# Optimization experiments

Measured on AMD Instinct MI355X. Metric: run time of the kernel, lower is better.

The kernel has to match this reference:

```python
import jax, jax.numpy as jnp
import numpy as np

TEMP = 10.0  # softmax_ called with N=10.0 in reduce_func

def qmul(a, b):
    # Hamilton product, rows are (w, x, y, z)
    aw, ax, ay, az = a[..., 0], a[..., 1], a[..., 2], a[..., 3]
    bw, bx, by, bz = b[..., 0], b[..., 1], b[..., 2], b[..., 3]
    return jnp.stack([
        aw * bw - ax * bx - ay * by - az * bz,
        aw * bx + ax * bw + ay * bz - az * by,
        aw * by - ax * bz + ay * bw + az * bx,
        aw * bz + ax * by - ay * bx + az * bw,
    ], axis=-1)

def setup_inputs() -> dict:
    key = jax.random.key(0)
    k1, k2, k3, k4, k5, k6 = jax.random.split(key, 6)
    N, E = 100000, 3200000
    node_levels = jax.random.uniform(k1, (N,), dtype=jnp.float32)
    node_q = jax.random.normal(k2, (N, 4), dtype=jnp.float32)
    node_q = node_q / jnp.linalg.norm(node_q, axis=1, keepdims=True)
    edge_rel_q = jax.random.normal(k3, (E, 4), dtype=jnp.float32)
    edge_rel_q = edge_rel_q / jnp.linalg.norm(edge_rel_q, axis=1, keepdims=True)
    edge_w = jax.random.uniform(k4, (E,), dtype=jnp.float32)
    src = jax.random.randint(k5, (E,), 0, N, dtype=jnp.int32)
    dst = jax.random.randint(k6, (E,), 0, N, dtype=jnp.int32)
    return {"node_levels": node_levels, "node_q": node_q,
            "edge_rel_q": edge_rel_q, "edge_w": edge_w,
            "src": src, "dst": dst}

def reference(node_levels, node_q, edge_rel_q, edge_w, src, dst):
    N = node_q.shape[0]
    # per-edge message: accumulated quaternion rel_q * q_src
    accu_q = qmul(edge_rel_q, node_q[src])          # [E,4]
    l_src = node_levels[src]                        # [E]
    # softmax logits: cost = w * l (self term has w = 1)
    cost_e = TEMP * edge_w * l_src                  # [E]
    cost_self = TEMP * node_levels                  # [N]
    # segmented stable softmax over {self} U in-edges per dst node
    seg_max = jax.ops.segment_max(cost_e, dst, num_segments=N)
    m = jnp.maximum(seg_max, cost_self)             # [N]
    exp_e = jnp.exp(cost_e - m[dst])                # [E]
    exp_self = jnp.exp(cost_self - m)               # [N]
    Z = jax.ops.segment_sum(exp_e, dst, num_segments=N) + exp_self
    # weighted sums
    sum_q = jax.ops.segment_sum(exp_e[:, None] * accu_q, dst, num_segments=N) \
            + exp_self[:, None] * node_q            # [N,4]
    sum_l = jax.ops.segment_sum(exp_e * l_src, dst, num_segments=N) \
            + exp_self * node_levels                # [N]
    out_q = sum_q / Z[:, None]
    out_levels = sum_l / Z
    # F.normalize(q, p=2, dim=1) with eps=1e-12 clamp
    norm = jnp.maximum(jnp.linalg.norm(out_q, axis=1, keepdims=True), 1e-12)
    return out_q / norm, out_levels
```

## Files before the change

kernel.cpp:

```cpp
#include <hip/hip_runtime.h>
#include <hip/hip_fp16.h>

#define TEMP 10.0f
#define TPB 512
#define HTPB 256
#define NBLK 768
#define SHIFT 9
#define GSZ 512
#define BMAX 256
#define TILE 2048
#define GTPB 1024
#define CAP 44

typedef float v2f  __attribute__((ext_vector_type(2)));
typedef float vf4  __attribute__((ext_vector_type(4)));
typedef unsigned uv4 __attribute__((ext_vector_type(4)));

__device__ __forceinline__ int   nt_i (const int* p)   { return __builtin_nontemporal_load(p); }
__device__ __forceinline__ float nt_f (const float* p) { return __builtin_nontemporal_load(p); }
__device__ __forceinline__ float4 nt_f4(const float4* p) {
    vf4 v = __builtin_nontemporal_load((const vf4*)p);
    return make_float4(v.x, v.y, v.z, v.w);
}
__device__ __forceinline__ uint4 nt_u4(const uint4* p) {
    uv4 v = __builtin_nontemporal_load((const uv4*)p);
    uint4 r; r.x = v.x; r.y = v.y; r.z = v.z; r.w = v.w; return r;
}

__device__ __forceinline__ void pk_fadd(float* p, float a, float b) {
#if __has_builtin(__builtin_amdgcn_global_atomic_fadd_v2f32)
    v2f v; v.x = a; v.y = b;
    __builtin_amdgcn_global_atomic_fadd_v2f32(
        (__attribute__((address_space(1))) v2f*)p, v);
#else
    atomicAdd(p, a); atomicAdd(p + 1, b);
#endif
}

__device__ __forceinline__ void hamilton(float4 a, float4 b,
                                         float& ow, float& ox, float& oy, float& oz) {
    ow = a.x*b.x - a.y*b.y - a.z*b.z - a.w*b.w;
    ox = a.x*b.y + a.y*b.x + a.z*b.w - a.w*b.z;
    oy = a.x*b.z - a.y*b.w + a.z*b.x + a.w*b.y;
    oz = a.x*b.w + a.y*b.z - a.z*b.y + a.w*b.x;
}

__device__ __forceinline__ unsigned f2h(float x) {
    return (unsigned)__half_as_ushort(__float2half_rn(x));
}
__device__ __forceinline__ float h2f(unsigned u) {
    return __half2float(__ushort_as_half((unsigned short)(u & 0xFFFFu)));
}

__global__ void __launch_bounds__(HTPB)
hist_kernel(const int* __restrict__ dst, unsigned* __restrict__ blkhist,
            int E, int B, int span) {
    extern __shared__ unsigned h[];
    for (int i = threadIdx.x; i < B; i += blockDim.x) h[i] = 0;
    __syncthreads();
    int start = blockIdx.x * span;
    int end = start + span; if (end > E) end = E;
    for (int e = start + threadIdx.x; e < end; e += blockDim.x)
        atomicAdd(&h[((unsigned)nt_i(&dst[e])) >> SHIFT], 1u);
    __syncthreads();
    for (int i = threadIdx.x; i < B; i += blockDim.x)
        blkhist[(size_t)i * gridDim.x + blockIdx.x] = h[i];
}

__global__ void __launch_bounds__(1024)
scan_blocks_kernel(unsigned* __restrict__ blkhist, unsigned* __restrict__ totals) {
    __shared__ unsigned s[1024];
    int b = blockIdx.x, t = threadIdx.x, n = blockDim.x;
    unsigned v = blkhist[(size_t)b * n + t];
    s[t] = v; __syncthreads();
    for (int off = 1; off < n; off <<= 1) {
        unsigned add = (t >= off) ? s[t - off] : 0u;
        __syncthreads();
        s[t] += add;
        __syncthreads();
    }
    blkhist[(size_t)b * n + t] = s[t] - v;
    if (t == n - 1) totals[b] = s[t];
}

__global__ void __launch_bounds__(1024)
scan_totals_kernel(const unsigned* __restrict__ totals,
                   unsigned* __restrict__ offsets, int B) {
    __shared__ unsigned s[1024];
    int t = threadIdx.x;
    unsigned v = (t < B) ? totals[t] : 0u;
    s[t] = v; __syncthreads();
    for (int off = 1; off < 1024; off <<= 1) {
        unsigned add = (t >= off) ? s[t - off] : 0u;
        __syncthreads();
        s[t] += add;
        __syncthreads();
    }
    if (t < B) offsets[t] = s[t] - v;
    if (t == B - 1) offsets[B] = s[t];
}

__global__ void __launch_bounds__(TPB)
scatter_sort_kernel(const float* __restrict__ nl, const float4* __restrict__ nq,
                    const float4* __restrict__ erq, const float* __restrict__ ew,
                    const int* __restrict__ src, const int* __restrict__ dst,
                    const unsigned* __restrict__ blkhist,
                    const unsigned* __restrict__ offsets,
                    uint4* __restrict__ buckets,
                    int E, int B, int span) {
    __shared__ uint4    stage[TILE];
    __shared__ unsigned gslot[TILE];
    __shared__ unsigned gcur[BMAX];
    __shared__ unsigned th[BMAX];
    __shared__ unsigned basec[BMAX];
    __shared__ unsigned curt[BMAX];

    int blk = blockIdx.x, nb = gridDim.x, tid = threadIdx.x;
    for (int b = tid; b < B; b += TPB)
        gcur[b] = offsets[b] + blkhist[(size_t)b * nb + blk];
    int start = blk * span;
    int end = start + span; if (end > E) end = E;

    for (int ts = start; ts < end; ts += TILE) {
        int tE = end - ts; if (tE > TILE) tE = TILE;
        for (int b = tid; b < B; b += TPB) th[b] = 0;
        __syncthreads();
        for (int k = tid; k < tE; k += TPB)
            atomicAdd(&th[((unsigned)dst[ts + k]) >> SHIFT], 1u);
        __syncthreads();
        if (tid < 64) {
            int lane = tid;
            unsigned vals[4];
            unsigned tot = 0;
            #pragma unroll
            for (int c = 0; c < 4; ++c) {
                int i = lane * 4 + c;
                vals[c] = (i < B) ? th[i] : 0u;
                tot += vals[c];
            }
            unsigned inc = tot;
            #pragma unroll
            for (int off = 1; off < 64; off <<= 1) {
                unsigned up = __shfl_up(inc, off);
                if (lane >= off) inc += up;
            }
            unsigned run = inc - tot;
            #pragma unroll
            for (int c = 0; c < 4; ++c) {
                int i = lane * 4 + c;
                if (i < B) { basec[i] = run; curt[i] = run; }
                run += vals[c];
            }
        }
        __syncthreads();
        for (int k = tid; k < tE; k += TPB) {
            int e = ts + k;
            int s_ = nt_i(&src[e]);
            unsigned d = (unsigned)dst[e];
            float l = nl[s_];
            float p = __expf(TEMP * nt_f(&ew[e]) * l);
            float ow, ox, oy, oz;
            hamilton(nt_f4(&erq[e]), nq[s_], ow, ox, oy, oz);
            unsigned b = d >> SHIFT;
            unsigned pos = atomicAdd(&curt[b], 1u);
            uint4 pk;
            pk.x = (d & (GSZ - 1)) | (f2h(p) << 16);
            pk.y = f2h(p * l)  | (f2h(p * ow) << 16);
            pk.z = f2h(p * ox) | (f2h(p * oy) << 16);
            pk.w = f2h(p * oz);
            stage[pos] = pk;
            gslot[pos] = gcur[b] + (pos - basec[b]);
        }
        __syncthreads();
        for (int k = tid; k < tE; k += TPB)
            buckets[gslot[k]] = stage[k];
        __syncthreads();
        for (int b = tid; b < B; b += TPB) gcur[b] += th[b];
        __syncthreads();
    }
}

__global__ void __launch_bounds__(GTPB)
gather_pay_kernel(const float* __restrict__ nl, const float4* __restrict__ nq,
                  const unsigned* __restrict__ offsets,
                  const uint4* __restrict__ buckets,
                  float4* __restrict__ out_q, float* __restrict__ out_l, int N) {
    __shared__ unsigned short idx[GSZ * CAP];
    __shared__ int   curn[GSZ];
    __shared__ float ovf[GSZ * 7];
    int b = blockIdx.x, tid = threadIdx.x;
    for (int i = tid; i < GSZ; i += GTPB) curn[i] = 0;
    for (int i = tid; i < GSZ * 7; i += GTPB) ovf[i] = 0.f;
    __syncthreads();

    unsigned s0 = offsets[b], s1 = offsets[b + 1];
    int M = (int)(s1 - s0);
    const unsigned* bx = (const unsigned*)(buckets + s0);

    for (int i = tid; i < M; i += GTPB) {
        unsigned w0 = bx[4 * (size_t)i];
        unsigned dl = w0 & (GSZ - 1);
        int slot = atomicAdd(&curn[dl], 1);
        if (slot < CAP) {
            idx[dl * CAP + slot] = (unsigned short)i;
        } else {
            uint4 pk = buckets[s0 + i];
            float* a = &ovf[dl * 7];
            atomicAdd(a + 0, h2f(pk.x >> 16));
            atomicAdd(a + 1, h2f(pk.y));
            atomicAdd(a + 2, h2f(pk.y >> 16));
            atomicAdd(a + 3, h2f(pk.z));
            atomicAdd(a + 4, h2f(pk.z >> 16));
            atomicAdd(a + 5, h2f(pk.w));
        }
    }
    __syncthreads();

    for (int half = 0; half < (GSZ * 4) / GTPB; ++half) {
        int j = half * (GTPB / 4) + (tid >> 2);
        int r = tid & 3;
        int deg = curn[j]; if (deg > CAP) deg = CAP;
        float aZ = 0.f, aL = 0.f, a0 = 0.f, a1 = 0.f, a2 = 0.f, a3 = 0.f;
        for (int s = r; s < deg; s += 4) {
            int i = idx[j * CAP + s];
            uint4 pk = nt_u4(&buckets[s0 + i]);
            aZ += h2f(pk.x >> 16);
            aL += h2f(pk.y);
            a0 += h2f(pk.y >> 16);
            a1 += h2f(pk.z);
            a2 += h2f(pk.z >> 16);
            a3 += h2f(pk.w);
        }
        for (int m = 1; m <= 2; m <<= 1) {
            aZ += __shfl_xor(aZ, m); aL += __shfl_xor(aL, m);
            a0 += __shfl_xor(a0, m); a1 += __shfl_xor(a1, m);
            a2 += __shfl_xor(a2, m); a3 += __shfl_xor(a3, m);
        }
        if (r == 0) {
            int n = b * GSZ + j;
            if (n < N) {
                const float* o = &ovf[j * 7];
                float l = nl[n];
                float ps = __expf(TEMP * l);
                float Z  = aZ + o[0] + ps;
                float sl = aL + o[1] + ps * l;
                float4 q = nq[n];
                float qw = a0 + o[2] + ps * q.x;
                float qx = a1 + o[3] + ps * q.y;
                float qy = a2 + o[4] + ps * q.z;
                float qz = a3 + o[5] + ps * q.w;
                float inv = 1.0f / Z;
                qw *= inv; qx *= inv; qy *= inv; qz *= inv;
                float norm = fmaxf(sqrtf(qw*qw + qx*qx + qy*qy + qz*qz), 1e-12f);
                float rn = 1.0f / norm;
                out_q[n] = make_float4(qw * rn, qx * rn, qy * rn, qz * rn);
                out_l[n] = sl * inv;
            }
        }
    }
}

__global__ void __launch_bounds__(256)
scatter_kernel(const int* __restrict__ dst, int* __restrict__ cnt,
               int* __restrict__ bucket, int cap,
               const float* __restrict__ node_levels, const float4* __restrict__ node_q,
               const float4* __restrict__ edge_rel_q, const float* __restrict__ edge_w,
               const int* __restrict__ src, float* __restrict__ side, int E) {
    int e = blockIdx.x * blockDim.x + threadIdx.x;
    if (e >= E) return;
    int d = dst[e];
    int slot = atomicAdd(&cnt[d], 1);
    if (slot < cap) {
        bucket[(long long)d * cap + slot] = e;
    } else {
        int s = src[e];
        float l = node_levels[s];
        float p = __expf(TEMP * edge_w[e] * l);
        float ow, ox, oy, oz;
        hamilton(edge_rel_q[e], node_q[s], ow, ox, oy, oz);
        float* rec = side + 6 * (long long)d;
        pk_fadd(rec + 0, p,      p * l);
        pk_fadd(rec + 2, p * ow, p * ox);
        pk_fadd(rec + 4, p * oy, p * oz);
    }
}

__global__ void __launch_bounds__(256)
gather_kernel(const float* __restrict__ node_levels, const float4* __restrict__ node_q,
              const float4* __restrict__ edge_rel_q, const float* __restrict__ edge_w,
              const int* __restrict__ src, const int* __restrict__ cnt,
              const int* __restrict__ bucket, int cap, const float* __restrict__ side,
              float4* __restrict__ out_q, float* __restrict__ out_l, int N) {
    int tid  = blockIdx.x * blockDim.x + threadIdx.x;
    int wave = tid >> 6, lane = tid & 63, half = lane >> 5, sub = lane & 31;
    int n = wave * 2 + half;
    float aZ = 0.f, aL = 0.f, a0 = 0.f, a1 = 0.f, a2 = 0.f, a3 = 0.f;
    if (n < N) {
        int deg = cnt[n]; if (deg > cap) deg = cap;
        const int* bkt = bucket + (long long)n * cap;
        for (int s = sub; s < deg; s += 32) {
            int e = bkt[s];
            int sn = src[e];
            float l = node_levels[sn];
            float p = __expf(TEMP * edge_w[e] * l);
            float ow, ox, oy, oz;
            hamilton(edge_rel_q[e], node_q[sn], ow, ox, oy, oz);
            aZ += p; aL += p * l; a0 += p * ow; a1 += p * ox; a2 += p * oy; a3 += p * oz;
        }
    }
    for (int m = 16; m; m >>= 1) {
        aZ += __shfl_xor(aZ, m); aL += __shfl_xor(aL, m);
        a0 += __shfl_xor(a0, m); a1 += __shfl_xor(a1, m);
        a2 += __shfl_xor(a2, m); a3 += __shfl_xor(a3, m);
    }
    if (sub == 0 && n < N) {
        const float* rec = side + 6 * (long long)n;
        float l  = node_levels[n];
        float ps = __expf(TEMP * l);
        float Z  = aZ + rec[0] + ps;
        float sl = aL + rec[1] + ps * l;
        float4 q = node_q[n];
        float qw = a0 + rec[2] + ps * q.x;
        float qx = a1 + rec[3] + ps * q.y;
        float qy = a2 + rec[4] + ps * q.z;
        float qz = a3 + rec[5] + ps * q.w;
        float inv = 1.0f / Z;
        qw *= inv; qx *= inv; qy *= inv; qz *= inv;
        float norm = fmaxf(sqrtf(qw*qw + qx*qx + qy*qy + qz*qz), 1e-12f);
        float rn = 1.0f / norm;
        out_q[n] = make_float4(qw * rn, qx * rn, qy * rn, qz * rn);
        out_l[n] = sl * inv;
    }
}

extern "C" void kernel_launch(void* const* d_in, const int* in_sizes, int n_in,
                              void* d_out, int out_size, void* d_ws, size_t ws_size,
                              hipStream_t stream) {
    const float*  node_levels = (const float*)d_in[0];
    const float4* node_q      = (const float4*)d_in[1];
    const float4* edge_rel_q  = (const float4*)d_in[2];
    const float*  edge_w      = (const float*)d_in[3];
    const int*    src         = (const int*)d_in[4];
    const int*    dst         = (const int*)d_in[5];

    const int N = in_sizes[0];
    const int E = in_sizes[3];

    const int B = (N + GSZ - 1) / GSZ;
    const int span = (E + NBLK - 1) / NBLK;

    size_t head_elems   = (size_t)B * NBLK + B + (B + 1);
    size_t buckets_byte = (head_elems * 4 + 15) & ~(size_t)15;
    size_t need         = buckets_byte + (size_t)E * 16;

    bool seg_ok = ((size_t)E / (size_t)B) < 32768;

    if (need <= ws_size && B <= BMAX && seg_ok) {
        unsigned* blkhist = (unsigned*)d_ws;
        unsigned* totals  = blkhist + (size_t)B * NBLK;
        unsigned* offsets = totals + B;
        uint4*    buckets = (uint4*)((char*)d_ws + buckets_byte);

        hist_kernel<<<NBLK, HTPB, B * 4, stream>>>(dst, blkhist, E, B, span);
        scan_blocks_kernel<<<B, NBLK, 0, stream>>>(blkhist, totals);
        scan_totals_kernel<<<1, 1024, 0, stream>>>(totals, offsets, B);
        scatter_sort_kernel<<<NBLK, TPB, 0, stream>>>(
            node_levels, node_q, edge_rel_q, edge_w, src, dst,
            blkhist, offsets, buckets, E, B, span);
        gather_pay_kernel<<<B, GTPB, 0, stream>>>(
            node_levels, node_q, offsets, buckets,
            (float4*)d_out, (float*)d_out + 4 * (long long)N, N);
    } else {
        const int tpb = 256;
        size_t cnt_elems  = ((size_t)N + 3) & ~(size_t)3;
        size_t side_elems = 6 * (size_t)N;
        size_t head_bytes = (cnt_elems + side_elems) * 4;
        int cap = 0;
        for (int c : {128, 64}) {
            if (head_bytes + (size_t)N * c * 4 <= ws_size) { cap = c; break; }
        }
        int*   cnt    = (int*)d_ws;
        float* side   = (float*)d_ws + cnt_elems;
        int*   bucket = (int*)d_ws + cnt_elems + side_elems;
        hipMemsetAsync(d_ws, 0, head_bytes, stream);
        scatter_kernel<<<(E + tpb - 1) / tpb, tpb, 0, stream>>>(
            dst, cnt, bucket, cap, node_levels, node_q, edge_rel_q, edge_w, src, side, E);
        int waves  = (N + 1) / 2;
        int blocks = (waves * 64 + tpb - 1) / tpb;
        gather_kernel<<<blocks, tpb, 0, stream>>>(
            node_levels, node_q, edge_rel_q, edge_w, src, cnt, bucket, cap, side,
            (float4*)d_out, (float*)d_out + 4 * (long long)N, N);
    }
}
```

Baseline: 237.6 us.

## Replace tiled LDS scatter sort with direct atomic bucket scatter and finer buckets

Drops the per-tile LDS histogram, scan and staging buffer in the scatter kernel. Each edge now claims its global bucket slot straight from a shared-memory cursor. Bucket size shrinks from 512 to 128 nodes, so there are about 782 buckets, more scatter blocks (1024), and gather blocks of 512 threads. This removes several barriers and an LDS round trip per tile, but the global writes are no longer coalesced within a bucket. It also adds more buckets and blocks to the histogram scans.

```diff
diff --git a/kernel.cpp b/kernel.cpp
--- a/kernel.cpp
+++ b/kernel.cpp
@@ -4,12 +4,11 @@
 #define TEMP 10.0f
 #define TPB 512
 #define HTPB 256
-#define NBLK 768
-#define SHIFT 9
-#define GSZ 512
-#define BMAX 256
-#define TILE 2048
-#define GTPB 1024
+#define NBLK 1024
+#define SHIFT 7
+#define GSZ 128
+#define BMAX 1024
+#define GTPB 512
 #define CAP 44
 
 typedef float v2f  __attribute__((ext_vector_type(2)));
@@ -101,82 +100,36 @@
 }
 
 __global__ void __launch_bounds__(TPB)
-scatter_sort_kernel(const float* __restrict__ nl, const float4* __restrict__ nq,
-                    const float4* __restrict__ erq, const float* __restrict__ ew,
-                    const int* __restrict__ src, const int* __restrict__ dst,
-                    const unsigned* __restrict__ blkhist,
-                    const unsigned* __restrict__ offsets,
-                    uint4* __restrict__ buckets,
-                    int E, int B, int span) {
-    __shared__ uint4    stage[TILE];
-    __shared__ unsigned gslot[TILE];
+scatter_direct_kernel(const float* __restrict__ nl, const float4* __restrict__ nq,
+                      const float4* __restrict__ erq, const float* __restrict__ ew,
+                      const int* __restrict__ src, const int* __restrict__ dst,
+                      const unsigned* __restrict__ blkhist,
+                      const unsigned* __restrict__ offsets,
+                      uint4* __restrict__ buckets,
+                      int E, int B, int span) {
     __shared__ unsigned gcur[BMAX];
-    __shared__ unsigned th[BMAX];
-    __shared__ unsigned basec[BMAX];
-    __shared__ unsigned curt[BMAX];
-
     int blk = blockIdx.x, nb = gridDim.x, tid = threadIdx.x;
     for (int b = tid; b < B; b += TPB)
         gcur[b] = offsets[b] + blkhist[(size_t)b * nb + blk];
+    __syncthreads();
     int start = blk * span;
     int end = start + span; if (end > E) end = E;
 
-    for (int ts = start; ts < end; ts += TILE) {
-        int tE = end - ts; if (tE > TILE) tE = TILE;
-        for (int b = tid; b < B; b += TPB) th[b] = 0;
-        __syncthreads();
-        for (int k = tid; k < tE; k += TPB)
-            atomicAdd(&th[((unsigned)dst[ts + k]) >> SHIFT], 1u);
-        __syncthreads();
-        if (tid < 64) {
-            int lane = tid;
-            unsigned vals[4];
-            unsigned tot = 0;
-            #pragma unroll
-            for (int c = 0; c < 4; ++c) {
-                int i = lane * 4 + c;
-                vals[c] = (i < B) ? th[i] : 0u;
-                tot += vals[c];
-            }
-            unsigned inc = tot;
-            #pragma unroll
-            for (int off = 1; off < 64; off <<= 1) {
-                unsigned up = __shfl_up(inc, off);
-                if (lane >= off) inc += up;
-            }
-            unsigned run = inc - tot;
-            #pragma unroll
-            for (int c = 0; c < 4; ++c) {
-                int i = lane * 4 + c;
-                if (i < B) { basec[i] = run; curt[i] = run; }
-                run += vals[c];
-            }
-        }
-        __syncthreads();
-        for (int k = tid; k < tE; k += TPB) {
-            int e = ts + k;
-            int s_ = nt_i(&src[e]);
-            unsigned d = (unsigned)dst[e];
-            float l = nl[s_];
-            float p = __expf(TEMP * nt_f(&ew[e]) * l);
-            float ow, ox, oy, oz;
-            hamilton(nt_f4(&erq[e]), nq[s_], ow, ox, oy, oz);
-            unsigned b = d >> SHIFT;
-            unsigned pos = atomicAdd(&curt[b], 1u);
-            uint4 pk;
-            pk.x = (d & (GSZ - 1)) | (f2h(p) << 16);
-            pk.y = f2h(p * l)  | (f2h(p * ow) << 16);
-            pk.z = f2h(p * ox) | (f2h(p * oy) << 16);
-            pk.w = f2h(p * oz);
-            stage[pos] = pk;
-            gslot[pos] = gcur[b] + (pos - basec[b]);
-        }
-        __syncthreads();
-        for (int k = tid; k < tE; k += TPB)
-            buckets[gslot[k]] = stage[k];
-        __syncthreads();
-        for (int b = tid; b < B; b += TPB) gcur[b] += th[b];
-        __syncthreads();
+    for (int e = start + tid; e < end; e += TPB) {
+        int s_ = nt_i(&src[e]);
+        unsigned d = (unsigned)nt_i(&dst[e]);
+        float l = nl[s_];
+        float p = __expf(TEMP * nt_f(&ew[e]) * l);
+        float ow, ox, oy, oz;
+        hamilton(nt_f4(&erq[e]), nq[s_], ow, ox, oy, oz);
+        unsigned b = d >> SHIFT;
+        unsigned slot = atomicAdd(&gcur[b], 1u);
+        uint4 pk;
+        pk.x = (d & (GSZ - 1)) | (f2h(p) << 16);
+        pk.y = f2h(p * l)  | (f2h(p * ow) << 16);
+        pk.z = f2h(p * ox) | (f2h(p * oy) << 16);
+        pk.w = f2h(p * oz);
+        buckets[slot] = pk;
     }
 }
 
@@ -364,7 +317,7 @@
         hist_kernel<<<NBLK, HTPB, B * 4, stream>>>(dst, blkhist, E, B, span);
         scan_blocks_kernel<<<B, NBLK, 0, stream>>>(blkhist, totals);
         scan_totals_kernel<<<1, 1024, 0, stream>>>(totals, offsets, B);
-        scatter_sort_kernel<<<NBLK, TPB, 0, stream>>>(
+        scatter_direct_kernel<<<NBLK, TPB, 0, stream>>>(
             node_levels, node_q, edge_rel_q, edge_w, src, dst,
             blkhist, offsets, buckets, E, B, span);
         gather_pay_kernel<<<B, GTPB, 0, stream>>>(
```

Measured after the change: 290.9 us. +22.4%, slower.

## Split per-bucket gather across blocks with shared atomics and separate finalize pass

Applied to the files above, without the earlier changes.

The gather stage now splits each destination bucket's edges across several blocks. Each block accumulates its share into shared memory with atomics, then adds its partial sums to a global side buffer with packed float atomics, and a new finalize kernel computes the softmax normalisation and output. This replaces the single-block-per-bucket index/overflow scheme, aiming for more parallelism (B is about 196, so few blocks ran before). The scatter kernel stores the bucket id in the packed record instead of a separate shared slot array, and NBLK is raised to 784. The cost is extra global atomics, a memset, and one more kernel launch.

```diff
diff --git a/kernel.cpp b/kernel.cpp
--- a/kernel.cpp
+++ b/kernel.cpp
@@ -4,13 +4,12 @@
 #define TEMP 10.0f
 #define TPB 512
 #define HTPB 256
-#define NBLK 768
+#define NBLK 784
 #define SHIFT 9
 #define GSZ 512
 #define BMAX 256
 #define TILE 2048
-#define GTPB 1024
-#define CAP 44
+#define GTPB 512
 
 typedef float v2f  __attribute__((ext_vector_type(2)));
 typedef float vf4  __attribute__((ext_vector_type(4)));
@@ -109,7 +108,6 @@
                     uint4* __restrict__ buckets,
                     int E, int B, int span) {
     __shared__ uint4    stage[TILE];
-    __shared__ unsigned gslot[TILE];
     __shared__ unsigned gcur[BMAX];
     __shared__ unsigned th[BMAX];
     __shared__ unsigned basec[BMAX];
@@ -167,13 +165,15 @@
             pk.x = (d & (GSZ - 1)) | (f2h(p) << 16);
             pk.y = f2h(p * l)  | (f2h(p * ow) << 16);
             pk.z = f2h(p * ox) | (f2h(p * oy) << 16);
-            pk.w = f2h(p * oz);
+            pk.w = f2h(p * oz) | (b << 16);
             stage[pos] = pk;
-            gslot[pos] = gcur[b] + (pos - basec[b]);
-        }
-        __syncthreads();
-        for (int k = tid; k < tE; k += TPB)
-            buckets[gslot[k]] = stage[k];
+        }
+        __syncthreads();
+        for (int k = tid; k < tE; k += TPB) {
+            uint4 pk = stage[k];
+            unsigned b = pk.w >> 16;
+            buckets[gcur[b] + ((unsigned)k - basec[b])] = pk;
+        }
         __syncthreads();
         for (int b = tid; b < B; b += TPB) gcur[b] += th[b];
         __syncthreads();
@@ -181,83 +181,67 @@
 }
 
 __global__ void __launch_bounds__(GTPB)
-gather_pay_kernel(const float* __restrict__ nl, const float4* __restrict__ nq,
-                  const unsigned* __restrict__ offsets,
+gather_acc_kernel(const unsigned* __restrict__ offsets,
                   const uint4* __restrict__ buckets,
-                  float4* __restrict__ out_q, float* __restrict__ out_l, int N) {
-    __shared__ unsigned short idx[GSZ * CAP];
-    __shared__ int   curn[GSZ];
-    __shared__ float ovf[GSZ * 7];
-    int b = blockIdx.x, tid = threadIdx.x;
-    for (int i = tid; i < GSZ; i += GTPB) curn[i] = 0;
-    for (int i = tid; i < GSZ * 7; i += GTPB) ovf[i] = 0.f;
+                  float* __restrict__ side, int N, int S) {
+    __shared__ float acc[GSZ * 7];
+    int b = blockIdx.x / S, part = blockIdx.x % S, tid = threadIdx.x;
+    for (int i = tid; i < GSZ * 7; i += GTPB) acc[i] = 0.f;
     __syncthreads();
 
     unsigned s0 = offsets[b], s1 = offsets[b + 1];
     int M = (int)(s1 - s0);
-    const unsigned* bx = (const unsigned*)(buckets + s0);
-
-    for (int i = tid; i < M; i += GTPB) {
-        unsigned w0 = bx[4 * (size_t)i];
-        unsigned dl = w0 & (GSZ - 1);
-        int slot = atomicAdd(&curn[dl], 1);
-        if (slot < CAP) {
-            idx[dl * CAP + slot] = (unsigned short)i;
-        } else {
-            uint4 pk = buckets[s0 + i];
-            float* a = &ovf[dl * 7];
-            atomicAdd(a + 0, h2f(pk.x >> 16));
-            atomicAdd(a + 1, h2f(pk.y));
-            atomicAdd(a + 2, h2f(pk.y >> 16));
-            atomicAdd(a + 3, h2f(pk.z));
-            atomicAdd(a + 4, h2f(pk.z >> 16));
-            atomicAdd(a + 5, h2f(pk.w));
-        }
+    int per = (M + S - 1) / S;
+    int r0 = part * per;
+    int r1 = r0 + per; if (r1 > M) r1 = M;
+
+    for (int i = r0 + tid; i < r1; i += GTPB) {
+        uint4 pk = nt_u4(&buckets[s0 + i]);
+        unsigned dl = pk.x & (GSZ - 1);
+        float* a = &acc[dl * 7];
+        atomicAdd(a + 0, h2f(pk.x >> 16));
+        atomicAdd(a + 1, h2f(pk.y));
+        atomicAdd(a + 2, h2f(pk.y >> 16));
+        atomicAdd(a + 3, h2f(pk.z));
+        atomicAdd(a + 4, h2f(pk.z >> 16));
+        atomicAdd(a + 5, h2f(pk.w));
     }
     __syncthreads();
 
-    for (int half = 0; half < (GSZ * 4) / GTPB; ++half) {
-        int j = half * (GTPB / 4) + (tid >> 2);
-        int r = tid & 3;
-        int deg = curn[j]; if (deg > CAP) deg = CAP;
-        float aZ = 0.f, aL = 0.f, a0 = 0.f, a1 = 0.f, a2 = 0.f, a3 = 0.f;
-        for (int s = r; s < deg; s += 4) {
-            int i = idx[j * CAP + s];
-            uint4 pk = nt_u4(&buckets[s0 + i]);
-            aZ += h2f(pk.x >> 16);
-            aL += h2f(pk.y);
-            a0 += h2f(pk.y >> 16);
-            a1 += h2f(pk.z);
-            a2 += h2f(pk.z >> 16);
-            a3 += h2f(pk.w);
-        }
-        for (int m = 1; m <= 2; m <<= 1) {
-            aZ += __shfl_xor(aZ, m); aL += __shfl_xor(aL, m);
-            a0 += __shfl_xor(a0, m); a1 += __shfl_xor(a1, m);
-            a2 += __shfl_xor(a2, m); a3 += __shfl_xor(a3, m);
-        }
-        if (r == 0) {
-            int n = b * GSZ + j;
-            if (n < N) {
-                const float* o = &ovf[j * 7];
-                float l = nl[n];
-                float ps = __expf(TEMP * l);
-                float Z  = aZ + o[0] + ps;
-                float sl = aL + o[1] + ps * l;
-                float4 q = nq[n];
-                float qw = a0 + o[2] + ps * q.x;
-                float qx = a1 + o[3] + ps * q.y;
-                float qy = a2 + o[4] + ps * q.z;
-                float qz = a3 + o[5] + ps * q.w;
-                float inv = 1.0f / Z;
-                qw *= inv; qx *= inv; qy *= inv; qz *= inv;
-                float norm = fmaxf(sqrtf(qw*qw + qx*qx + qy*qy + qz*qz), 1e-12f);
-                float rn = 1.0f / norm;
-                out_q[n] = make_float4(qw * rn, qx * rn, qy * rn, qz * rn);
-                out_l[n] = sl * inv;
-            }
-        }
-    }
+    int j = tid;
+    int n = b * GSZ + j;
+    if (j < GSZ && n < N) {
+        float* sp = side + (size_t)n * 6;
+        const float* a = &acc[j * 7];
+        pk_fadd(sp + 0, a[0], a[1]);
+        pk_fadd(sp + 2, a[2], a[3]);
+        pk_fadd(sp + 4, a[4], a[5]);
+    }
+}
+
+__global__ void __launch_bounds__(256)
+finalize_kernel(const float* __restrict__ nl, const float4* __restrict__ nq,
+                const float* __restrict__ side,
+                float4* __restrict__ out_q, float* __restrict__ out_l, int N) {
+    int n = blockIdx.x * 256 + threadIdx.x;
+    if (n >= N) return;
+    const float2* sp = (const float2*)(side + (size_t)n * 6);
+    float2 s0 = sp[0], s1 = sp[1], s2 = sp[2];
+    float l  = nl[n];
+    float ps = __expf(TEMP * l);
+    float Z  = s0.x + ps;
+    float sl = s0.y + ps * l;
+    float4 q = nq[n];
+    float qw = s1.x + ps * q.x;
+    float qx = s1.y + ps * q.y;
+    float qy = s2.x + ps * q.z;
+    float qz = s2.y + ps * q.w;
+    float inv = 1.0f / Z;
+    qw *= inv; qx *= inv; qy *= inv; qz *= inv;
+    float norm = fmaxf(sqrtf(qw*qw + qx*qx + qy*qy + qz*qz), 1e-12f);
+    float rn = 1.0f / norm;
+    out_q[n] = make_float4(qw * rn, qx * rn, qy * rn, qz * rn);
+    out_l[n] = sl * inv;
 }
 
 __global__ void __launch_bounds__(256)
@@ -351,25 +335,28 @@
 
     size_t head_elems   = (size_t)B * NBLK + B + (B + 1);
     size_t buckets_byte = (head_elems * 4 + 15) & ~(size_t)15;
-    size_t need         = buckets_byte + (size_t)E * 16;
-
-    bool seg_ok = ((size_t)E / (size_t)B) < 32768;
-
-    if (need <= ws_size && B <= BMAX && seg_ok) {
+    size_t side_byte    = buckets_byte + (size_t)E * 16;
+    size_t need         = side_byte + (size_t)N * 24;
+
+    if (need <= ws_size && B <= BMAX) {
         unsigned* blkhist = (unsigned*)d_ws;
         unsigned* totals  = blkhist + (size_t)B * NBLK;
         unsigned* offsets = totals + B;
         uint4*    buckets = (uint4*)((char*)d_ws + buckets_byte);
-
+        float*    side    = (float*)((char*)d_ws + side_byte);
+
+        int S = (1024 + B - 1) / B;
+
+        hipMemsetAsync(side, 0, (size_t)N * 24, stream);
         hist_kernel<<<NBLK, HTPB, B * 4, stream>>>(dst, blkhist, E, B, span);
         scan_blocks_kernel<<<B, NBLK, 0, stream>>>(blkhist, totals);
         scan_totals_kernel<<<1, 1024, 0, stream>>>(totals, offsets, B);
         scatter_sort_kernel<<<NBLK, TPB, 0, stream>>>(
             node_levels, node_q, edge_rel_q, edge_w, src, dst,
             blkhist, offsets, buckets, E, B, span);
-        gather_pay_kernel<<<B, GTPB, 0, stream>>>(
-            node_levels, node_q, offsets, buckets,
-            (float4*)d_out, (float*)d_out + 4 * (long long)N, N);
+        gather_acc_kernel<<<B * S, GTPB, 0, stream>>>(offsets, buckets, side, N, S);
+        finalize_kernel<<<(N + 255) / 256, 256, 0, stream>>>(
+            node_levels, node_q, side, (float4*)d_out, (float*)d_out + 4 * (long long)N, N);
     } else {
         const int tpb = 256;
         size_t cnt_elems  = ((size_t)N + 3) & ~(size_t)3;
```

Measured after the change: 327.3 us. 37.8% more time.
